# Optimization experiments

Measured on AMD Instinct MI355X. Metric: run time of the kernel, lower is better.

The kernel has to match this reference:

```python
import jax, jax.numpy as jnp
import numpy as np

N_NODES = 12288
N_FEATURES = 256
KEY_DIM = 128
N_GRAPHS = 192


def setup_inputs() -> dict:
    key = jax.random.key(0)
    k1, k2, k3, k4, k5 = jax.random.split(key, 5)
    node_out = jax.random.normal(k1, (N_NODES, N_FEATURES), dtype=jnp.float32)
    batch = jnp.sort(jax.random.randint(k2, (N_NODES,), 0, N_GRAPHS, dtype=jnp.int64))
    # xavier_uniform: limit = sqrt(6 / (fan_in + fan_out))
    lim_qk = float(np.sqrt(6.0 / (N_FEATURES + KEY_DIM)))
    lim_v = float(np.sqrt(6.0 / (N_FEATURES + N_FEATURES)))
    query_weight = jax.random.uniform(k3, (N_FEATURES, KEY_DIM), jnp.float32, -lim_qk, lim_qk)
    key_weight = jax.random.uniform(k4, (N_FEATURES, KEY_DIM), jnp.float32, -lim_qk, lim_qk)
    value_weight = jax.random.uniform(k5, (N_FEATURES, N_FEATURES), jnp.float32, -lim_v, lim_v)
    return {
        "node_out": node_out,
        "batch": batch,
        "query_weight": query_weight,
        "key_weight": key_weight,
        "value_weight": value_weight,
    }


def reference(node_out, batch, query_weight, key_weight, value_weight):
    n_features = node_out.shape[1]
    Q = node_out @ query_weight            # [N, K]
    K = node_out @ key_weight              # [N, K]
    V = node_out @ value_weight            # [N, F]
    # NOTE: original scales by sqrt(n_features), not sqrt(key_dim)
    scores = (Q @ K.T) / jnp.sqrt(jnp.asarray(n_features, dtype=Q.dtype))  # [N, N]
    mask = batch[:, None] == batch[None, :]  # block-diagonal per-graph mask
    scores = jnp.where(mask, scores, -jnp.inf)
    attn = jax.nn.softmax(scores, axis=-1)   # every row has >=1 valid entry
    context = attn @ V                        # [N, F]
    return jax.ops.segment_sum(context, batch, num_segments=N_GRAPHS)  # [G, F]
```

## Files before the change

kernel.cpp:

```cpp
#include <hip/hip_runtime.h>
#include <hip/hip_bf16.h>

#define N_NODES  12288
#define N_FEAT   256
#define KDIM     128
#define N_GRAPHS 192
#define NMAX     112
#define KSTRIDE_U 68
#define XS_STRIDE_U 132

#define WS_STARTS 0
#define WS_WBUF   1024
#define WS_QB     (WS_WBUF + N_NODES * 4)
#define WS_KB     (WS_QB + N_NODES * 64 * 4)
#define WS_WT     (WS_KB + N_NODES * 64 * 4)

typedef __bf16 bf16x8 __attribute__((ext_vector_type(8)));
typedef float  f32x4  __attribute__((ext_vector_type(4)));

__device__ __forceinline__ unsigned bf16_rne(float f) {
  unsigned u = __float_as_uint(f);
  return (u + 0x7FFFu + ((u >> 16) & 1u)) >> 16;
}
__device__ __forceinline__ unsigned pack_bf16(float lo, float hi) {
  return bf16_rne(lo) | (bf16_rne(hi) << 16);
}
__device__ __forceinline__ float bf_lo(unsigned u) { return __uint_as_float(u << 16); }
__device__ __forceinline__ float bf_hi(unsigned u) { return __uint_as_float(u & 0xFFFF0000u); }

__global__ __launch_bounds__(64) void wt_prep_k(const float* __restrict__ Wq,
                                                const float* __restrict__ Wk,
                                                const int* __restrict__ batch,
                                                unsigned* __restrict__ Wt,
                                                int* __restrict__ starts) {
  const int n = blockIdx.x;
  const int t = threadIdx.x;
  const float* src = (n < KDIM) ? (Wq + n) : (Wk + (n - KDIM));
  float f0 = src[(4 * t + 0) * KDIM];
  float f1 = src[(4 * t + 1) * KDIM];
  float f2 = src[(4 * t + 2) * KDIM];
  float f3 = src[(4 * t + 3) * KDIM];
  Wt[n * 128 + 2 * t]     = pack_bf16(f0, f1);
  Wt[n * 128 + 2 * t + 1] = pack_bf16(f2, f3);

  if (t == 0 && n <= N_GRAPHS) {
    int lo = 0, hi = N_NODES;
    while (lo < hi) {
      int mid = (lo + hi) >> 1;
      if (batch[mid] < n) lo = mid + 1; else hi = mid;
    }
    starts[n] = lo;
  }
}

__global__ __launch_bounds__(256) void qk_proj_k(const float* __restrict__ X,
                                                 const unsigned* __restrict__ Wt,
                                                 unsigned* __restrict__ Qb,
                                                 unsigned* __restrict__ Kb) {
  __shared__ unsigned Xs_u[16 * XS_STRIDE_U];

  const int tid  = threadIdx.x;
  const int lane = tid & 63;
  const int wv   = tid >> 6;
  const int r0   = blockIdx.x * 16;
  const int l15  = lane & 15;
  const int quad = lane >> 4;

  {
    const int row = tid >> 4, seg = tid & 15;
    const float* xp = &X[(size_t)(r0 + row) * N_FEAT + seg * 16];
    float4 a = *(const float4*)xp;
    float4 b = *(const float4*)(xp + 4);
    float4 c = *(const float4*)(xp + 8);
    float4 d = *(const float4*)(xp + 12);
    unsigned* dst = &Xs_u[row * XS_STRIDE_U + seg * 8];
    *(uint4*)dst       = make_uint4(pack_bf16(a.x, a.y), pack_bf16(a.z, a.w),
                                    pack_bf16(b.x, b.y), pack_bf16(b.z, b.w));
    *(uint4*)(dst + 4) = make_uint4(pack_bf16(c.x, c.y), pack_bf16(c.z, c.w),
                                    pack_bf16(d.x, d.y), pack_bf16(d.z, d.w));
  }
  __syncthreads();

  f32x4 acc[4];
#pragma unroll
  for (int ni = 0; ni < 4; ni++) acc[ni] = (f32x4){0.f, 0.f, 0.f, 0.f};

#pragma unroll
  for (int ks = 0; ks < 8; ks++) {
    bf16x8 a = *(const bf16x8*)&Xs_u[l15 * XS_STRIDE_U + ks * 16 + quad * 4];
    bf16x8 b[4];
#pragma unroll
    for (int ni = 0; ni < 4; ni++)
      b[ni] = *(const bf16x8*)&Wt[(size_t)(wv * 64 + ni * 16 + l15) * 128 + ks * 16 + quad * 4];
#pragma unroll
    for (int ni = 0; ni < 4; ni++)
      acc[ni] = __builtin_amdgcn_mfma_f32_16x16x32_bf16(a, b[ni], acc[ni], 0, 0, 0);
  }

  unsigned* dst = (wv < 2) ? Qb : Kb;
  const float scale = (wv < 2) ? 0.0625f : 1.0f;
  const int colbase = (wv & 1) * 64;
#pragma unroll
  for (int ni = 0; ni < 4; ni++) {
    const int col = colbase + ni * 16 + l15;
#pragma unroll
    for (int e = 0; e < 4; e++) {
      const int row = r0 + quad * 4 + e;
      unsigned b = bf16_rne(acc[ni][e] * scale);
      unsigned partner = __shfl_xor((int)b, 1);
      if ((lane & 1) == 0)
        dst[row * 64 + (col >> 1)] = b | (partner << 16);
    }
  }
}

__global__ __launch_bounds__(512) void attn_pool_k(const float* __restrict__ X,
                                                   const int* __restrict__ starts,
                                                   const unsigned* __restrict__ Qb,
                                                   const unsigned* __restrict__ Kb,
                                                   const float* __restrict__ Wv,
                                                   float* __restrict__ out,
                                                   float* __restrict__ wbuf) {
  __shared__ unsigned Ks_u[NMAX * KSTRIDE_U];
  __shared__ float    w_lds[8][NMAX];
  __shared__ float    red[2][256];
  __shared__ float    Us[256];

  const int tid  = threadIdx.x;
  const int lane = tid & 63;
  const int wv   = tid >> 6;
  const int l15  = lane & 15;
  const int quad = lane >> 4;
  const int g    = blockIdx.x;

  const int i0 = starts[g];
  const int n  = starts[g + 1] - i0;
  const float BIG = 1e30f;
  const bool fast = (n <= NMAX);

  if (fast) {
    for (int idx = tid; idx < n * 16; idx += 512) {
      int j = idx >> 4, c = idx & 15;
      *(uint4*)&Ks_u[j * KSTRIDE_U + 4 * c] = *(const uint4*)&Kb[(size_t)(i0 + j) * 64 + 4 * c];
    }
    __syncthreads();

    float wl[7];
#pragma unroll
    for (int f = 0; f < 7; f++) wl[f] = 0.f;

    const int ns = (n + 15) >> 4;
    if (wv < ns) {
      const int s = wv;
      const int arow = min(s * 16 + l15, n - 1);
      const unsigned* qrow = &Qb[(size_t)(i0 + arow) * 64];
      bf16x8 au[4];
#pragma unroll
      for (int ks = 0; ks < 4; ks++)
        au[ks] = *(const bf16x8*)&qrow[ks * 16 + quad * 4];

      f32x4 acc[7];
#pragma unroll
      for (int f = 0; f < 7; f++) acc[f] = (f32x4){0.f, 0.f, 0.f, 0.f};
#pragma unroll
      for (int f = 0; f < 7; f++) {
#pragma unroll
        for (int ks = 0; ks < 4; ks++) {
          bf16x8 bu = *(const bf16x8*)&Ks_u[(f * 16 + l15) * KSTRIDE_U + ks * 16 + quad * 4];
          acc[f] = __builtin_amdgcn_mfma_f32_16x16x32_bf16(au[ks], bu, acc[f], 0, 0, 0);
        }
      }
#pragma unroll
      for (int f = 0; f < 7; f++)
        if (f * 16 + l15 >= n) {
          acc[f][0] = -BIG; acc[f][1] = -BIG; acc[f][2] = -BIG; acc[f][3] = -BIG;
        }

#pragma unroll
      for (int e = 0; e < 4; e++) {
        float m = -BIG;
#pragma unroll
        for (int f = 0; f < 7; f++) m = fmaxf(m, acc[f][e]);
        m = fmaxf(m, __shfl_xor(m, 1));
        m = fmaxf(m, __shfl_xor(m, 2));
        m = fmaxf(m, __shfl_xor(m, 4));
        m = fmaxf(m, __shfl_xor(m, 8));
        float p[7], l = 0.f;
#pragma unroll
        for (int f = 0; f < 7; f++) { p[f] = __expf(acc[f][e] - m); l += p[f]; }
        l += __shfl_xor(l, 1);
        l += __shfl_xor(l, 2);
        l += __shfl_xor(l, 4);
        l += __shfl_xor(l, 8);
        const int row = s * 16 + quad * 4 + e;
        float inv = (row < n) ? (1.f / l) : 0.f;
#pragma unroll
        for (int f = 0; f < 7; f++) wl[f] = fmaf(p[f], inv, wl[f]);
      }
    }

#pragma unroll
    for (int f = 0; f < 7; f++) {
      wl[f] += __shfl_xor(wl[f], 16);
      wl[f] += __shfl_xor(wl[f], 32);
    }
    if (lane < 16) {
#pragma unroll
      for (int f = 0; f < 7; f++) w_lds[wv][f * 16 + lane] = wl[f];
    }
    __syncthreads();

    if (tid < NMAX) {
      float t = 0.f;
#pragma unroll
      for (int k = 0; k < 8; k++) t += w_lds[k][tid];
      w_lds[0][tid] = t;
    }
    __syncthreads();
  } else {
    for (int idx = tid; idx < n; idx += 512) wbuf[i0 + idx] = 0.f;
    __syncthreads();
    for (int lr = wv; lr < n; lr += 8) {
      const uint4* qp4 = (const uint4*)&Qb[(size_t)(i0 + lr) * 64];
      float m_run = -BIG, l_run = 0.f;
      for (int jb = 0; jb < n; jb += 64) {
        int j = jb + lane;
        int jc = min(j, n - 1);
        const uint4* kp4 = (const uint4*)&Kb[(size_t)(i0 + jc) * 64];
        float s = 0.f;
        for (int c = 0; c < 16; c++) {
          uint4 Q1 = qp4[c];
          uint4 K1 = kp4[c];
          s = fmaf(bf_lo(Q1.x), bf_lo(K1.x), s); s = fmaf(bf_hi(Q1.x), bf_hi(K1.x), s);
          s = fmaf(bf_lo(Q1.y), bf_lo(K1.y), s); s = fmaf(bf_hi(Q1.y), bf_hi(K1.y), s);
          s = fmaf(bf_lo(Q1.z), bf_lo(K1.z), s); s = fmaf(bf_hi(Q1.z), bf_hi(K1.z), s);
          s = fmaf(bf_lo(Q1.w), bf_lo(K1.w), s); s = fmaf(bf_hi(Q1.w), bf_hi(K1.w), s);
        }
        if (j >= n) s = -BIG;
        float mc = s;
        for (int off = 32; off; off >>= 1) mc = fmaxf(mc, __shfl_xor(mc, off));
        float m_new = fmaxf(m_run, mc);
        float lc = __expf(s - m_new);
        for (int off = 32; off; off >>= 1) lc += __shfl_xor(lc, off);
        l_run = l_run * __expf(m_run - m_new) + lc;
        m_run = m_new;
      }
      float inv = 1.f / l_run;
      for (int jb = 0; jb < n; jb += 64) {
        int j = jb + lane;
        int jc = min(j, n - 1);
        const uint4* kp4 = (const uint4*)&Kb[(size_t)(i0 + jc) * 64];
        float s = 0.f;
        for (int c = 0; c < 16; c++) {
          uint4 Q1 = qp4[c];
          uint4 K1 = kp4[c];
          s = fmaf(bf_lo(Q1.x), bf_lo(K1.x), s); s = fmaf(bf_hi(Q1.x), bf_hi(K1.x), s);
          s = fmaf(bf_lo(Q1.y), bf_lo(K1.y), s); s = fmaf(bf_hi(Q1.y), bf_hi(K1.y), s);
          s = fmaf(bf_lo(Q1.z), bf_lo(K1.z), s); s = fmaf(bf_hi(Q1.z), bf_hi(K1.z), s);
          s = fmaf(bf_lo(Q1.w), bf_lo(K1.w), s); s = fmaf(bf_hi(Q1.w), bf_hi(K1.w), s);
        }
        if (j < n) atomicAdd(&wbuf[i0 + j], __expf(s - m_run) * inv);
      }
    }
    __threadfence();
    __syncthreads();
  }

  const int f  = tid & 255;
  const int jp = tid >> 8;
  float ua = 0.f, ub = 0.f;
  if (fast) {
    int j = jp;
    for (; j + 2 < n; j += 4) {
      ua = fmaf(w_lds[0][j],     X[(size_t)(i0 + j) * N_FEAT + f], ua);
      ub = fmaf(w_lds[0][j + 2], X[(size_t)(i0 + j + 2) * N_FEAT + f], ub);
    }
    for (; j < n; j += 2)
      ua = fmaf(w_lds[0][j], X[(size_t)(i0 + j) * N_FEAT + f], ua);
  } else {
    for (int j = jp; j < n; j += 2) {
      float wj = atomicAdd(&wbuf[i0 + j], 0.f);
      ua = fmaf(wj, X[(size_t)(i0 + j) * N_FEAT + f], ua);
    }
  }
  red[jp][f] = ua + ub;
  __syncthreads();
  if (jp == 0) Us[f] = red[0][f] + red[1][f];
  __syncthreads();

  const int k0 = jp * 128;
  const float* wp = Wv + (size_t)k0 * N_FEAT + f;
  const float* us = &Us[k0];
  float a0 = 0.f, a1 = 0.f, a2 = 0.f, a3 = 0.f;
#pragma unroll 8
  for (int k = 0; k < 128; k += 4) {
    a0 = fmaf(us[k],     wp[(size_t)k * N_FEAT], a0);
    a1 = fmaf(us[k + 1], wp[(size_t)(k + 1) * N_FEAT], a1);
    a2 = fmaf(us[k + 2], wp[(size_t)(k + 2) * N_FEAT], a2);
    a3 = fmaf(us[k + 3], wp[(size_t)(k + 3) * N_FEAT], a3);
  }
  __syncthreads();
  red[jp][f] = (a0 + a1) + (a2 + a3);
  __syncthreads();
  if (jp == 0) out[g * N_FEAT + f] = red[0][f] + red[1][f];
}

extern "C" void kernel_launch(void* const* d_in, const int* in_sizes, int n_in,
                              void* d_out, int out_size, void* d_ws, size_t ws_size,
                              hipStream_t stream) {
  const float* X     = (const float*)d_in[0];
  const int*   batch = (const int*)d_in[1];
  const float* Wq    = (const float*)d_in[2];
  const float* Wk    = (const float*)d_in[3];
  const float* Wv    = (const float*)d_in[4];
  float* out = (float*)d_out;

  char* ws = (char*)d_ws;
  int*      starts = (int*)(ws + WS_STARTS);
  float*    wbuf   = (float*)(ws + WS_WBUF);
  unsigned* Qb     = (unsigned*)(ws + WS_QB);
  unsigned* Kb     = (unsigned*)(ws + WS_KB);
  unsigned* Wt     = (unsigned*)(ws + WS_WT);

  wt_prep_k<<<256, 64, 0, stream>>>(Wq, Wk, batch, Wt, starts);
  qk_proj_k<<<N_NODES / 16, 256, 0, stream>>>(X, Wt, Qb, Kb);
  attn_pool_k<<<N_GRAPHS, 512, 0, stream>>>(X, starts, Qb, Kb, Wv, out, wbuf);
}
```

Before: 98.17 us.

## Split attention pooling across feature quarters and move Wv projection to separate kernel

The single per-graph attention+pool kernel is split into two kernels. The first launches four blocks per graph, each redundantly computing the softmax column weights but pooling only a 64-feature slice of X into U. The second applies Wv with two blocks per graph. This gives more blocks than the 192 of the old launch, in exchange for recomputing the attention scores four times and paying for an extra launch plus a global round-trip of U.

```diff
diff --git a/kernel.cpp b/kernel.cpp
--- a/kernel.cpp
+++ b/kernel.cpp
@@ -10,8 +10,9 @@
 #define XS_STRIDE_U 132
 
 #define WS_STARTS 0
-#define WS_WBUF   1024
-#define WS_QB     (WS_WBUF + N_NODES * 4)
+#define WS_U      1024
+#define WS_WSLOW  (WS_U + N_GRAPHS * N_FEAT * 4)
+#define WS_QB     (WS_WSLOW + 4 * N_NODES * 4)
 #define WS_KB     (WS_QB + N_NODES * 64 * 4)
 #define WS_WT     (WS_KB + N_NODES * 64 * 4)
 
@@ -114,29 +115,29 @@
   }
 }
 
-__global__ __launch_bounds__(512) void attn_pool_k(const float* __restrict__ X,
-                                                   const int* __restrict__ starts,
-                                                   const unsigned* __restrict__ Qb,
-                                                   const unsigned* __restrict__ Kb,
-                                                   const float* __restrict__ Wv,
-                                                   float* __restrict__ out,
-                                                   float* __restrict__ wbuf) {
+__global__ __launch_bounds__(512) void attn_u_k(const float* __restrict__ X,
+                                                const int* __restrict__ starts,
+                                                const unsigned* __restrict__ Qb,
+                                                const unsigned* __restrict__ Kb,
+                                                float* __restrict__ U,
+                                                float* __restrict__ wslow) {
   __shared__ unsigned Ks_u[NMAX * KSTRIDE_U];
   __shared__ float    w_lds[8][NMAX];
-  __shared__ float    red[2][256];
-  __shared__ float    Us[256];
+  __shared__ float    red[8][64];
 
   const int tid  = threadIdx.x;
   const int lane = tid & 63;
   const int wv   = tid >> 6;
   const int l15  = lane & 15;
   const int quad = lane >> 4;
-  const int g    = blockIdx.x;
+  const int g    = blockIdx.x >> 2;
+  const int qi   = blockIdx.x & 3;
 
   const int i0 = starts[g];
   const int n  = starts[g + 1] - i0;
   const float BIG = 1e30f;
   const bool fast = (n <= NMAX);
+  float* seg = wslow + (size_t)qi * N_NODES;
 
   if (fast) {
     for (int idx = tid; idx < n * 16; idx += 512) {
@@ -218,7 +219,7 @@
     }
     __syncthreads();
   } else {
-    for (int idx = tid; idx < n; idx += 512) wbuf[i0 + idx] = 0.f;
+    for (int idx = tid; idx < n; idx += 512) seg[i0 + idx] = 0.f;
     __syncthreads();
     for (int lr = wv; lr < n; lr += 8) {
       const uint4* qp4 = (const uint4*)&Qb[(size_t)(i0 + lr) * 64];
@@ -259,50 +260,71 @@
           s = fmaf(bf_lo(Q1.z), bf_lo(K1.z), s); s = fmaf(bf_hi(Q1.z), bf_hi(K1.z), s);
           s = fmaf(bf_lo(Q1.w), bf_lo(K1.w), s); s = fmaf(bf_hi(Q1.w), bf_hi(K1.w), s);
         }
-        if (j < n) atomicAdd(&wbuf[i0 + j], __expf(s - m_run) * inv);
+        if (j < n) atomicAdd(&seg[i0 + j], __expf(s - m_run) * inv);
       }
     }
     __threadfence();
     __syncthreads();
   }
 
-  const int f  = tid & 255;
-  const int jp = tid >> 8;
+  const int fl = tid & 63;
+  const int f  = qi * 64 + fl;
+  const int jp = tid >> 6;
   float ua = 0.f, ub = 0.f;
   if (fast) {
     int j = jp;
-    for (; j + 2 < n; j += 4) {
+    for (; j + 8 < n; j += 16) {
       ua = fmaf(w_lds[0][j],     X[(size_t)(i0 + j) * N_FEAT + f], ua);
-      ub = fmaf(w_lds[0][j + 2], X[(size_t)(i0 + j + 2) * N_FEAT + f], ub);
-    }
-    for (; j < n; j += 2)
+      ub = fmaf(w_lds[0][j + 8], X[(size_t)(i0 + j + 8) * N_FEAT + f], ub);
+    }
+    for (; j < n; j += 8)
       ua = fmaf(w_lds[0][j], X[(size_t)(i0 + j) * N_FEAT + f], ua);
   } else {
-    for (int j = jp; j < n; j += 2) {
-      float wj = atomicAdd(&wbuf[i0 + j], 0.f);
+    for (int j = jp; j < n; j += 8) {
+      float wj = atomicAdd(&seg[i0 + j], 0.f);
       ua = fmaf(wj, X[(size_t)(i0 + j) * N_FEAT + f], ua);
     }
   }
-  red[jp][f] = ua + ub;
+  red[jp][fl] = ua + ub;
   __syncthreads();
-  if (jp == 0) Us[f] = red[0][f] + red[1][f];
+  if (tid < 64) {
+    float t = 0.f;
+#pragma unroll
+    for (int k = 0; k < 8; k++) t += red[k][tid];
+    U[g * N_FEAT + qi * 64 + tid] = t;
+  }
+}
+
+__global__ __launch_bounds__(512) void vout_o_k(const float* __restrict__ U,
+                                                const float* __restrict__ Wv,
+                                                float* __restrict__ out) {
+  __shared__ float Us[256];
+  __shared__ float part[4][128];
+  const int g   = blockIdx.x >> 1;
+  const int fh  = blockIdx.x & 1;
+  const int tid = threadIdx.x;
+  const int fl  = tid & 127;
+  const int f   = fh * 128 + fl;
+  const int kq  = tid >> 7;
+
+  if (tid < 256) Us[tid] = U[g * N_FEAT + tid];
   __syncthreads();
 
-  const int k0 = jp * 128;
+  const int k0 = kq * 64;
   const float* wp = Wv + (size_t)k0 * N_FEAT + f;
   const float* us = &Us[k0];
   float a0 = 0.f, a1 = 0.f, a2 = 0.f, a3 = 0.f;
-#pragma unroll 8
-  for (int k = 0; k < 128; k += 4) {
+#pragma unroll 4
+  for (int k = 0; k < 64; k += 4) {
     a0 = fmaf(us[k],     wp[(size_t)k * N_FEAT], a0);
     a1 = fmaf(us[k + 1], wp[(size_t)(k + 1) * N_FEAT], a1);
     a2 = fmaf(us[k + 2], wp[(size_t)(k + 2) * N_FEAT], a2);
     a3 = fmaf(us[k + 3], wp[(size_t)(k + 3) * N_FEAT], a3);
   }
+  part[kq][fl] = (a0 + a1) + (a2 + a3);
   __syncthreads();
-  red[jp][f] = (a0 + a1) + (a2 + a3);
-  __syncthreads();
-  if (jp == 0) out[g * N_FEAT + f] = red[0][f] + red[1][f];
+  if (kq == 0)
+    out[g * N_FEAT + f] = (part[0][fl] + part[1][fl]) + (part[2][fl] + part[3][fl]);
 }
 
 extern "C" void kernel_launch(void* const* d_in, const int* in_sizes, int n_in,
@@ -317,12 +339,14 @@
 
   char* ws = (char*)d_ws;
   int*      starts = (int*)(ws + WS_STARTS);
-  float*    wbuf   = (float*)(ws + WS_WBUF);
+  float*    U      = (float*)(ws + WS_U);
+  float*    wslow  = (float*)(ws + WS_WSLOW);
   unsigned* Qb     = (unsigned*)(ws + WS_QB);
   unsigned* Kb     = (unsigned*)(ws + WS_KB);
   unsigned* Wt     = (unsigned*)(ws + WS_WT);
 
   wt_prep_k<<<256, 64, 0, stream>>>(Wq, Wk, batch, Wt, starts);
   qk_proj_k<<<N_NODES / 16, 256, 0, stream>>>(X, Wt, Qb, Kb);
-  attn_pool_k<<<N_GRAPHS, 512, 0, stream>>>(X, starts, Qb, Kb, Wv, out, wbuf);
-}
+  attn_u_k<<<N_GRAPHS * 4, 512, 0, stream>>>(X, starts, Qb, Kb, U, wslow);
+  vout_o_k<<<N_GRAPHS * 2, 512, 0, stream>>>(U, Wv, out);
+}
```

Measured after the change: 99.47 us. About the same (+1.3%).

## Fuse Q/K projection into per-graph attention kernel via LDS

Applied to the files above, without the earlier changes.

Removes the separate Q/K projection kernel. Each graph's block now computes bf16 Q and K for its own rows with MFMA, writes them to shared memory, and immediately computes scores and softmax weights from them. This drops the global round trip for Q/K and one kernel launch. In exchange only 192 blocks do the projection work, with up to 7 waves each, so parallelism for the projection is much lower than the previous 768-block kernel. The rare oversized-graph fallback recomputes Q/K in fp32 scalar code.

```diff
diff --git a/kernel.cpp b/kernel.cpp
--- a/kernel.cpp
+++ b/kernel.cpp
@@ -6,17 +6,19 @@
 #define KDIM     128
 #define N_GRAPHS 192
 #define NMAX     112
-#define KSTRIDE_U 68
-#define XS_STRIDE_U 132
+#define KSTR     68
+#define QSTR     66
 
 #define WS_STARTS 0
-#define WS_WBUF   1024
-#define WS_QB     (WS_WBUF + N_NODES * 4)
-#define WS_KB     (WS_QB + N_NODES * 64 * 4)
-#define WS_WT     (WS_KB + N_NODES * 64 * 4)
+#define WS_WGLOB  1024
+#define WS_QSLOW  (WS_WGLOB + N_NODES * 4)
+#define WS_KSLOW  (WS_QSLOW + N_NODES * KDIM * 4)
+#define WS_WT     (WS_KSLOW + N_NODES * KDIM * 4)
 
 typedef __bf16 bf16x8 __attribute__((ext_vector_type(8)));
 typedef float  f32x4  __attribute__((ext_vector_type(4)));
+
+union U8 { unsigned u[4]; bf16x8 v; };
 
 __device__ __forceinline__ unsigned bf16_rne(float f) {
   unsigned u = __float_as_uint(f);
@@ -25,8 +27,6 @@
 __device__ __forceinline__ unsigned pack_bf16(float lo, float hi) {
   return bf16_rne(lo) | (bf16_rne(hi) << 16);
 }
-__device__ __forceinline__ float bf_lo(unsigned u) { return __uint_as_float(u << 16); }
-__device__ __forceinline__ float bf_hi(unsigned u) { return __uint_as_float(u & 0xFFFF0000u); }
 
 __global__ __launch_bounds__(64) void wt_prep_k(const float* __restrict__ Wq,
                                                 const float* __restrict__ Wk,
@@ -53,78 +53,20 @@
   }
 }
 
-__global__ __launch_bounds__(256) void qk_proj_k(const float* __restrict__ X,
-                                                 const unsigned* __restrict__ Wt,
-                                                 unsigned* __restrict__ Qb,
-                                                 unsigned* __restrict__ Kb) {
-  __shared__ unsigned Xs_u[16 * XS_STRIDE_U];
-
-  const int tid  = threadIdx.x;
-  const int lane = tid & 63;
-  const int wv   = tid >> 6;
-  const int r0   = blockIdx.x * 16;
-  const int l15  = lane & 15;
-  const int quad = lane >> 4;
-
-  {
-    const int row = tid >> 4, seg = tid & 15;
-    const float* xp = &X[(size_t)(r0 + row) * N_FEAT + seg * 16];
-    float4 a = *(const float4*)xp;
-    float4 b = *(const float4*)(xp + 4);
-    float4 c = *(const float4*)(xp + 8);
-    float4 d = *(const float4*)(xp + 12);
-    unsigned* dst = &Xs_u[row * XS_STRIDE_U + seg * 8];
-    *(uint4*)dst       = make_uint4(pack_bf16(a.x, a.y), pack_bf16(a.z, a.w),
-                                    pack_bf16(b.x, b.y), pack_bf16(b.z, b.w));
-    *(uint4*)(dst + 4) = make_uint4(pack_bf16(c.x, c.y), pack_bf16(c.z, c.w),
-                                    pack_bf16(d.x, d.y), pack_bf16(d.z, d.w));
-  }
-  __syncthreads();
-
-  f32x4 acc[4];
-#pragma unroll
-  for (int ni = 0; ni < 4; ni++) acc[ni] = (f32x4){0.f, 0.f, 0.f, 0.f};
-
-#pragma unroll
-  for (int ks = 0; ks < 8; ks++) {
-    bf16x8 a = *(const bf16x8*)&Xs_u[l15 * XS_STRIDE_U + ks * 16 + quad * 4];
-    bf16x8 b[4];
-#pragma unroll
-    for (int ni = 0; ni < 4; ni++)
-      b[ni] = *(const bf16x8*)&Wt[(size_t)(wv * 64 + ni * 16 + l15) * 128 + ks * 16 + quad * 4];
-#pragma unroll
-    for (int ni = 0; ni < 4; ni++)
-      acc[ni] = __builtin_amdgcn_mfma_f32_16x16x32_bf16(a, b[ni], acc[ni], 0, 0, 0);
-  }
-
-  unsigned* dst = (wv < 2) ? Qb : Kb;
-  const float scale = (wv < 2) ? 0.0625f : 1.0f;
-  const int colbase = (wv & 1) * 64;
-#pragma unroll
-  for (int ni = 0; ni < 4; ni++) {
-    const int col = colbase + ni * 16 + l15;
-#pragma unroll
-    for (int e = 0; e < 4; e++) {
-      const int row = r0 + quad * 4 + e;
-      unsigned b = bf16_rne(acc[ni][e] * scale);
-      unsigned partner = __shfl_xor((int)b, 1);
-      if ((lane & 1) == 0)
-        dst[row * 64 + (col >> 1)] = b | (partner << 16);
-    }
-  }
-}
-
-__global__ __launch_bounds__(512) void attn_pool_k(const float* __restrict__ X,
-                                                   const int* __restrict__ starts,
-                                                   const unsigned* __restrict__ Qb,
-                                                   const unsigned* __restrict__ Kb,
-                                                   const float* __restrict__ Wv,
-                                                   float* __restrict__ out,
-                                                   float* __restrict__ wbuf) {
-  __shared__ unsigned Ks_u[NMAX * KSTRIDE_U];
-  __shared__ float    w_lds[8][NMAX];
+__global__ __launch_bounds__(512) void attn_fused_k(const float* __restrict__ X,
+                                                    const int* __restrict__ starts,
+                                                    const unsigned* __restrict__ Wt,
+                                                    const float* __restrict__ Wq,
+                                                    const float* __restrict__ Wk,
+                                                    const float* __restrict__ Wv,
+                                                    float* __restrict__ out,
+                                                    float* __restrict__ wglob,
+                                                    float* __restrict__ Qslow,
+                                                    float* __restrict__ Kslow) {
+  __shared__ unsigned Ks_u[NMAX * KSTR];
+  __shared__ unsigned Qs_u[NMAX * QSTR];
+  __shared__ float    w_lds[7][NMAX];
   __shared__ float    red[2][256];
-  __shared__ float    Us[256];
 
   const int tid  = threadIdx.x;
   const int lane = tid & 63;
@@ -139,26 +81,68 @@
   const bool fast = (n <= NMAX);
 
   if (fast) {
-    for (int idx = tid; idx < n * 16; idx += 512) {
-      int j = idx >> 4, c = idx & 15;
-      *(uint4*)&Ks_u[j * KSTRIDE_U + 4 * c] = *(const uint4*)&Kb[(size_t)(i0 + j) * 64 + 4 * c];
-    }
-    __syncthreads();
-
-    float wl[7];
-#pragma unroll
-    for (int f = 0; f < 7; f++) wl[f] = 0.f;
-
     const int ns = (n + 15) >> 4;
+
     if (wv < ns) {
       const int s = wv;
-      const int arow = min(s * 16 + l15, n - 1);
-      const unsigned* qrow = &Qb[(size_t)(i0 + arow) * 64];
+      const int arow = i0 + min(s * 16 + l15, n - 1);
+      f32x4 accq[8], acck[8];
+#pragma unroll
+      for (int nt = 0; nt < 8; nt++) {
+        accq[nt] = (f32x4){0.f, 0.f, 0.f, 0.f};
+        acck[nt] = (f32x4){0.f, 0.f, 0.f, 0.f};
+      }
+#pragma unroll
+      for (int ks = 0; ks < 8; ks++) {
+        const float* xp = &X[(size_t)arow * N_FEAT + ks * 32 + quad * 8];
+        float4 xa = *(const float4*)xp;
+        float4 xb = *(const float4*)(xp + 4);
+        U8 t;
+        t.u[0] = pack_bf16(xa.x, xa.y); t.u[1] = pack_bf16(xa.z, xa.w);
+        t.u[2] = pack_bf16(xb.x, xb.y); t.u[3] = pack_bf16(xb.z, xb.w);
+        bf16x8 a = t.v;
+#pragma unroll
+        for (int nt = 0; nt < 8; nt++) {
+          bf16x8 bq = *(const bf16x8*)&Wt[(size_t)(nt * 16 + l15) * 128 + ks * 16 + quad * 4];
+          bf16x8 bk = *(const bf16x8*)&Wt[(size_t)(128 + nt * 16 + l15) * 128 + ks * 16 + quad * 4];
+          accq[nt] = __builtin_amdgcn_mfma_f32_16x16x32_bf16(a, bq, accq[nt], 0, 0, 0);
+          acck[nt] = __builtin_amdgcn_mfma_f32_16x16x32_bf16(a, bk, acck[nt], 0, 0, 0);
+        }
+      }
+#pragma unroll
+      for (int nt = 0; nt < 8; nt++) {
+        const int c = nt * 16 + l15;
+#pragma unroll
+        for (int e = 0; e < 4; e++) {
+          const int r = s * 16 + quad * 4 + e;
+          unsigned bq = bf16_rne(accq[nt][e] * 0.0625f);
+          unsigned bk = bf16_rne(acck[nt][e]);
+          unsigned bqp = __shfl_xor((int)bq, 1);
+          unsigned bkp = __shfl_xor((int)bk, 1);
+          if ((lane & 1) == 0) {
+            Qs_u[r * QSTR + (c >> 1)] = bq | (bqp << 16);
+            Ks_u[r * KSTR + (c >> 1)] = bk | (bkp << 16);
+          }
+        }
+      }
+    }
+    __syncthreads();
+
+    float wl[7];
+#pragma unroll
+    for (int f = 0; f < 7; f++) wl[f] = 0.f;
+
+    if (wv < ns) {
+      const int s = wv;
       bf16x8 au[4];
 #pragma unroll
-      for (int ks = 0; ks < 4; ks++)
-        au[ks] = *(const bf16x8*)&qrow[ks * 16 + quad * 4];
-
+      for (int ks = 0; ks < 4; ks++) {
+        U8 t;
+        const unsigned* qp = &Qs_u[(s * 16 + l15) * QSTR + ks * 16 + quad * 4];
+        *(uint2*)&t.u[0] = *(const uint2*)qp;
+        *(uint2*)&t.u[2] = *(const uint2*)(qp + 2);
+        au[ks] = t.v;
+      }
       f32x4 acc[7];
 #pragma unroll
       for (int f = 0; f < 7; f++) acc[f] = (f32x4){0.f, 0.f, 0.f, 0.f};
@@ -166,7 +150,7 @@
       for (int f = 0; f < 7; f++) {
 #pragma unroll
         for (int ks = 0; ks < 4; ks++) {
-          bf16x8 bu = *(const bf16x8*)&Ks_u[(f * 16 + l15) * KSTRIDE_U + ks * 16 + quad * 4];
+          bf16x8 bu = *(const bf16x8*)&Ks_u[(f * 16 + l15) * KSTR + ks * 16 + quad * 4];
           acc[f] = __builtin_amdgcn_mfma_f32_16x16x32_bf16(au[ks], bu, acc[f], 0, 0, 0);
         }
       }
@@ -175,7 +159,6 @@
         if (f * 16 + l15 >= n) {
           acc[f][0] = -BIG; acc[f][1] = -BIG; acc[f][2] = -BIG; acc[f][3] = -BIG;
         }
-
 #pragma unroll
       for (int e = 0; e < 4; e++) {
         float m = -BIG;
@@ -198,13 +181,12 @@
         for (int f = 0; f < 7; f++) wl[f] = fmaf(p[f], inv, wl[f]);
       }
     }
-
 #pragma unroll
     for (int f = 0; f < 7; f++) {
       wl[f] += __shfl_xor(wl[f], 16);
       wl[f] += __shfl_xor(wl[f], 32);
     }
-    if (lane < 16) {
+    if (wv < 7 && lane < 16) {
 #pragma unroll
       for (int f = 0; f < 7; f++) w_lds[wv][f * 16 + lane] = wl[f];
     }
@@ -213,29 +195,36 @@
     if (tid < NMAX) {
       float t = 0.f;
 #pragma unroll
-      for (int k = 0; k < 8; k++) t += w_lds[k][tid];
+      for (int k = 0; k < 7; k++) t += w_lds[k][tid];
       w_lds[0][tid] = t;
     }
     __syncthreads();
   } else {
-    for (int idx = tid; idx < n; idx += 512) wbuf[i0 + idx] = 0.f;
+    for (int idx = tid; idx < n; idx += 512) wglob[i0 + idx] = 0.f;
+    __syncthreads();
+    for (int r = tid >> 7; r < n; r += 4) {
+      const int kd = tid & 127;
+      const float* xr = &X[(size_t)(i0 + r) * N_FEAT];
+      float aq = 0.f, ak = 0.f;
+      for (int k = 0; k < N_FEAT; k++) {
+        float xv = xr[k];
+        aq = fmaf(xv, Wq[k * KDIM + kd], aq);
+        ak = fmaf(xv, Wk[k * KDIM + kd], ak);
+      }
+      Qslow[(size_t)(i0 + r) * KDIM + kd] = aq * 0.0625f;
+      Kslow[(size_t)(i0 + r) * KDIM + kd] = ak;
+    }
+    __threadfence();
     __syncthreads();
     for (int lr = wv; lr < n; lr += 8) {
-      const uint4* qp4 = (const uint4*)&Qb[(size_t)(i0 + lr) * 64];
+      const float* qp = &Qslow[(size_t)(i0 + lr) * KDIM];
       float m_run = -BIG, l_run = 0.f;
       for (int jb = 0; jb < n; jb += 64) {
         int j = jb + lane;
         int jc = min(j, n - 1);
-        const uint4* kp4 = (const uint4*)&Kb[(size_t)(i0 + jc) * 64];
+        const float* kp = &Kslow[(size_t)(i0 + jc) * KDIM];
         float s = 0.f;
-        for (int c = 0; c < 16; c++) {
-          uint4 Q1 = qp4[c];
-          uint4 K1 = kp4[c];
-          s = fmaf(bf_lo(Q1.x), bf_lo(K1.x), s); s = fmaf(bf_hi(Q1.x), bf_hi(K1.x), s);
-          s = fmaf(bf_lo(Q1.y), bf_lo(K1.y), s); s = fmaf(bf_hi(Q1.y), bf_hi(K1.y), s);
-          s = fmaf(bf_lo(Q1.z), bf_lo(K1.z), s); s = fmaf(bf_hi(Q1.z), bf_hi(K1.z), s);
-          s = fmaf(bf_lo(Q1.w), bf_lo(K1.w), s); s = fmaf(bf_hi(Q1.w), bf_hi(K1.w), s);
-        }
+        for (int k = 0; k < KDIM; k++) s = fmaf(qp[k], kp[k], s);
         if (j >= n) s = -BIG;
         float mc = s;
         for (int off = 32; off; off >>= 1) mc = fmaxf(mc, __shfl_xor(mc, off));
@@ -249,17 +238,10 @@
       for (int jb = 0; jb < n; jb += 64) {
         int j = jb + lane;
         int jc = min(j, n - 1);
-        const uint4* kp4 = (const uint4*)&Kb[(size_t)(i0 + jc) * 64];
+        const float* kp = &Kslow[(size_t)(i0 + jc) * KDIM];
         float s = 0.f;
-        for (int c = 0; c < 16; c++) {
-          uint4 Q1 = qp4[c];
-          uint4 K1 = kp4[c];
-          s = fmaf(bf_lo(Q1.x), bf_lo(K1.x), s); s = fmaf(bf_hi(Q1.x), bf_hi(K1.x), s);
-          s = fmaf(bf_lo(Q1.y), bf_lo(K1.y), s); s = fmaf(bf_hi(Q1.y), bf_hi(K1.y), s);
-          s = fmaf(bf_lo(Q1.z), bf_lo(K1.z), s); s = fmaf(bf_hi(Q1.z), bf_hi(K1.z), s);
-          s = fmaf(bf_lo(Q1.w), bf_lo(K1.w), s); s = fmaf(bf_hi(Q1.w), bf_hi(K1.w), s);
-        }
-        if (j < n) atomicAdd(&wbuf[i0 + j], __expf(s - m_run) * inv);
+        for (int k = 0; k < KDIM; k++) s = fmaf(qp[k], kp[k], s);
+        if (j < n) atomicAdd(&wglob[i0 + j], __expf(s - m_run) * inv);
       }
     }
     __threadfence();
@@ -279,18 +261,18 @@
       ua = fmaf(w_lds[0][j], X[(size_t)(i0 + j) * N_FEAT + f], ua);
   } else {
     for (int j = jp; j < n; j += 2) {
-      float wj = atomicAdd(&wbuf[i0 + j], 0.f);
+      float wj = atomicAdd(&wglob[i0 + j], 0.f);
       ua = fmaf(wj, X[(size_t)(i0 + j) * N_FEAT + f], ua);
     }
   }
   red[jp][f] = ua + ub;
   __syncthreads();
-  if (jp == 0) Us[f] = red[0][f] + red[1][f];
+  if (jp == 0) red[0][f] += red[1][f];
   __syncthreads();
 
   const int k0 = jp * 128;
   const float* wp = Wv + (size_t)k0 * N_FEAT + f;
-  const float* us = &Us[k0];
+  const float* us = &red[0][k0];
   float a0 = 0.f, a1 = 0.f, a2 = 0.f, a3 = 0.f;
 #pragma unroll 8
   for (int k = 0; k < 128; k += 4) {
@@ -299,10 +281,11 @@
     a2 = fmaf(us[k + 2], wp[(size_t)(k + 2) * N_FEAT], a2);
     a3 = fmaf(us[k + 3], wp[(size_t)(k + 3) * N_FEAT], a3);
   }
+  float* op = (float*)w_lds;
   __syncthreads();
-  red[jp][f] = (a0 + a1) + (a2 + a3);
+  op[jp * 256 + f] = (a0 + a1) + (a2 + a3);
   __syncthreads();
-  if (jp == 0) out[g * N_FEAT + f] = red[0][f] + red[1][f];
+  if (jp == 0) out[g * N_FEAT + f] = op[f] + op[256 + f];
 }
 
 extern "C" void kernel_launch(void* const* d_in, const int* in_sizes, int n_in,
@@ -317,12 +300,12 @@
 
   char* ws = (char*)d_ws;
   int*      starts = (int*)(ws + WS_STARTS);
-  float*    wbuf   = (float*)(ws + WS_WBUF);
-  unsigned* Qb     = (unsigned*)(ws + WS_QB);
-  unsigned* Kb     = (unsigned*)(ws + WS_KB);
+  float*    wglob  = (float*)(ws + WS_WGLOB);
+  float*    Qslow  = (float*)(ws + WS_QSLOW);
+  float*    Kslow  = (float*)(ws + WS_KSLOW);
   unsigned* Wt     = (unsigned*)(ws + WS_WT);
 
   wt_prep_k<<<256, 64, 0, stream>>>(Wq, Wk, batch, Wt, starts);
-  qk_proj_k<<<N_NODES / 16, 256, 0, stream>>>(X, Wt, Qb, Kb);
-  attn_pool_k<<<N_GRAPHS, 512, 0, stream>>>(X, starts, Qb, Kb, Wv, out, wbuf);
-}
+  attn_fused_k<<<N_GRAPHS, 512, 0, stream>>>(X, starts, Wt, Wq, Wk, Wv,
+                                             out, wglob, Qslow, Kslow);
+}
```

Result: slower. 104.3 us (+6.2%).
